# Optimization experiments

Measured on AMD Instinct MI355X. Metric: run time of the kernel, lower is better.

## Reference

```python
import jax, jax.numpy as jnp
import numpy as np


def setup_inputs() -> dict:
    key = jax.random.key(0)
    ks = jax.random.split(key, 9)
    B, C, H, W = 8, 512, 56, 56
    E = 256  # embed_dim = in_channels / r
    s = 0.02
    return {
        "x": jax.random.normal(ks[0], (B, C, H, W), dtype=jnp.float32),
        "wq": jax.random.normal(ks[1], (E, C), dtype=jnp.float32) * s,
        "bq": jax.random.normal(ks[2], (E,), dtype=jnp.float32) * s,
        "wk": jax.random.normal(ks[3], (E, C), dtype=jnp.float32) * s,
        "bk": jax.random.normal(ks[4], (E,), dtype=jnp.float32) * s,
        "wv": jax.random.normal(ks[5], (E, C), dtype=jnp.float32) * s,
        "bv": jax.random.normal(ks[6], (E,), dtype=jnp.float32) * s,
        "wo": jax.random.normal(ks[7], (C, E), dtype=jnp.float32) * s,
        "bo": jax.random.normal(ks[8], (C,), dtype=jnp.float32) * s,
    }


def reference(x, wq, bq, wk, bk, wv, bv, wo, bo):
    B, C, H, W = x.shape
    N = H * W
    # 1x1 convs == per-pixel linear projections; flatten spatial dims
    xf = x.reshape(B, C, N)                                   # b c n
    q = jnp.einsum("ec,bcn->bne", wq, xf) + bq                # b n e
    k = jnp.einsum("ec,bcn->ben", wk, xf) + bk[None, :, None] # b e n
    v = jnp.einsum("ec,bcn->bne", wv, xf) + bv                # b n e
    attn = jnp.einsum("bne,bem->bnm", q, k) / N               # b n n (unnormalized, /N scale)
    embed = jnp.einsum("bnm,bme->bne", attn, v)               # b n e
    out = jnp.einsum("ce,bne->bcn", wo, embed) + bo[None, :, None]
    return out.reshape(B, C, H, W) + x
```

## Files before the change

kernel.cpp:

```cpp
#include <hip/hip_runtime.h>
#include <hip/hip_bf16.h>


typedef __attribute__((ext_vector_type(8))) __bf16 bf16x8;
typedef __attribute__((ext_vector_type(4))) float floatx4;

struct __align__(8) bh4 { __hip_bfloat16 x, y, z, w; };
struct __align__(16) bh8 { __hip_bfloat16 h[8]; };

__device__ __forceinline__ void load_lds16(const void* g, void* l) {
    __builtin_amdgcn_global_load_lds((const __attribute__((address_space(1))) void*)g,
                                     (__attribute__((address_space(3))) void*)l, 16, 0, 0);
}

__global__ __launch_bounds__(256)
void prep_all(const float* __restrict__ wo, const float* __restrict__ wv,
              const float* __restrict__ wq, const float* __restrict__ wk,
              const float* __restrict__ bq, const float* __restrict__ bk,
              const float* __restrict__ bv,
              __hip_bfloat16* __restrict__ Pdb, __hip_bfloat16* __restrict__ Qtb,
              float* __restrict__ u, float* __restrict__ r, float* __restrict__ w,
              float* __restrict__ kap, float* __restrict__ sv)
{
    const int tid = threadIdx.x;
    if (blockIdx.z == 2) {
        int blk = blockIdx.y * 8 + blockIdx.x;
        if (blk < 2) {
            int c = blk * 256 + tid;
            float su = 0.f, sr = 0.f, sw = 0.f;
            for (int e = 0; e < 256; ++e) {
                su = fmaf(wo[(long long)c * 256 + e], bv[e], su);
                sr = fmaf(bk[e], wq[(long long)e * 512 + c], sr);
                sw = fmaf(wk[(long long)e * 512 + c], bq[e], sw);
            }
            u[c] = su; r[c] = sr; w[c] = sw;
            if (c == 0) {
                float k2 = 0.f;
                for (int e = 0; e < 256; ++e) k2 = fmaf(bk[e], bq[e], k2);
                *kap = k2;
            }
        } else if (blk == 2) {
            float4* p = (float4*)sv;
            for (int i = tid; i < 1024; i += 256) p[i] = make_float4(0.f, 0.f, 0.f, 0.f);
        }
        return;
    }
    __shared__ __align__(16) float As[16][68];
    __shared__ __align__(16) float Bs[16][68];
    const int tx = tid & 15, ty = tid >> 4;
    const int m0 = blockIdx.y * 64, n0 = blockIdx.x * 64;
    const bool doQ = (blockIdx.z == 1);
    const int lk = tid >> 4, lc = (tid & 15) * 4;
    const int lr = tid >> 2, lk4 = (tid & 3) * 4;
    float acc[4][4] = {};
    for (int k0 = 0; k0 < 256; k0 += 16) {
        float4 av, bv4;
        if (doQ) {
            av = *(const float4*)&wq[(long long)(k0 + lk) * 512 + m0 + lc];
            bv4 = *(const float4*)&wk[(long long)(k0 + lk) * 512 + n0 + lc];
        } else {
            av = *(const float4*)&wo[(long long)(m0 + lr) * 256 + k0 + lk4];
            bv4 = *(const float4*)&wv[(long long)(k0 + lk) * 512 + n0 + lc];
        }
        __syncthreads();
        if (doQ) {
            *(float4*)&As[lk][lc] = av;
        } else {
            As[lk4 + 0][lr] = av.x; As[lk4 + 1][lr] = av.y;
            As[lk4 + 2][lr] = av.z; As[lk4 + 3][lr] = av.w;
        }
        *(float4*)&Bs[lk][lc] = bv4;
        __syncthreads();
#pragma unroll
        for (int kk = 0; kk < 16; ++kk) {
            float a[4], b[4];
#pragma unroll
            for (int i = 0; i < 4; ++i) { a[i] = As[kk][ty * 4 + i]; b[i] = Bs[kk][tx * 4 + i]; }
#pragma unroll
            for (int i = 0; i < 4; ++i)
#pragma unroll
                for (int j = 0; j < 4; ++j) acc[i][j] = fmaf(a[i], b[j], acc[i][j]);
        }
    }
    const int mo = m0 + ty * 4, no = n0 + tx * 4;
    if (doQ) {
#pragma unroll
        for (int i = 0; i < 4; ++i)
#pragma unroll
            for (int j = 0; j < 4; ++j)
                Qtb[(long long)(mo + i) * 512 + no + j] = __float2bfloat16(acc[i][j]);
    } else {
#pragma unroll
        for (int i = 0; i < 4; ++i)
#pragma unroll
            for (int j = 0; j < 4; ++j) {
                __hip_bfloat16 v = __float2bfloat16(acc[i][j]);
                Pdb[(long long)(mo + i) * 1024 + no + j] = v;
                Pdb[(long long)(mo + i) * 1024 + no + j + 512] = v;
            }
    }
}

__global__ __launch_bounds__(256)
void transpose_conv(const float* __restrict__ x, __hip_bfloat16* __restrict__ xT,
                    __hip_bfloat16* __restrict__ xnp, float* __restrict__ s)
{
    __shared__ float t[64][65];
    const int b = blockIdx.z;
    const int n0 = blockIdx.x * 64, c0 = blockIdx.y * 64;
    const int tid = threadIdx.x;
    const int nch = tid & 7;
    const int cr  = tid >> 3;
    __hip_bfloat16* xTo = xT + (long long)b * 3200 * 512;
    __hip_bfloat16* xno = xnp + (long long)b * 512 * 3200;

    if (n0 >= 3136) {
        bh8 z8;
#pragma unroll
        for (int k = 0; k < 8; ++k) z8.h[k] = __float2bfloat16(0.f);
#pragma unroll
        for (int pass = 0; pass < 2; ++pass) {
            int rr = cr + 32 * pass;
            *(bh8*)&xno[(long long)(c0 + rr) * 3200 + n0 + nch * 8] = z8;
            *(bh8*)&xTo[(long long)(n0 + rr) * 512 + c0 + nch * 8] = z8;
        }
        return;
    }
    const float* xb = x + (long long)b * 512 * 3136;
#pragma unroll
    for (int pass = 0; pass < 2; ++pass) {
        const int cl = cr + 32 * pass;
        const int c = c0 + cl;
        const float* xr = xb + (long long)c * 3136 + n0 + nch * 8;
        float4 v0 = *(const float4*)xr;
        float4 v1 = *(const float4*)(xr + 4);
        bh8 o;
        o.h[0] = __float2bfloat16(v0.x); o.h[1] = __float2bfloat16(v0.y);
        o.h[2] = __float2bfloat16(v0.z); o.h[3] = __float2bfloat16(v0.w);
        o.h[4] = __float2bfloat16(v1.x); o.h[5] = __float2bfloat16(v1.y);
        o.h[6] = __float2bfloat16(v1.z); o.h[7] = __float2bfloat16(v1.w);
        *(bh8*)&xno[(long long)c * 3200 + n0 + nch * 8] = o;
        const int nl = nch * 8;
        t[nl + 0][cl] = v0.x; t[nl + 1][cl] = v0.y;
        t[nl + 2][cl] = v0.z; t[nl + 3][cl] = v0.w;
        t[nl + 4][cl] = v1.x; t[nl + 5][cl] = v1.y;
        t[nl + 6][cl] = v1.z; t[nl + 7][cl] = v1.w;
        float rs = v0.x + v0.y + v0.z + v0.w + v1.x + v1.y + v1.z + v1.w;
        rs += __shfl_xor(rs, 1, 8);
        rs += __shfl_xor(rs, 2, 8);
        rs += __shfl_xor(rs, 4, 8);
        if (nch == 0) atomicAdd(&s[b * 512 + c], rs);
    }
    __syncthreads();
#pragma unroll
    for (int pass = 0; pass < 2; ++pass) {
        const int nl = cr + 32 * pass;
        const int cc = nch * 8;
        bh8 o;
#pragma unroll
        for (int k = 0; k < 8; ++k) o.h[k] = __float2bfloat16(t[nl][cc + k]);
        *(bh8*)&xTo[(long long)(n0 + nl) * 512 + c0 + cc] = o;
    }
}

__global__ __launch_bounds__(256)
void vec2_kernel(const __hip_bfloat16* __restrict__ T, const __hip_bfloat16* __restrict__ Pdb,
                 const __hip_bfloat16* __restrict__ Qtb, const float* __restrict__ s,
                 const float* __restrict__ u, const float* __restrict__ w,
                 const float* __restrict__ kap, const float* __restrict__ bo,
                 float* __restrict__ ps, float* __restrict__ sq, float* __restrict__ a2)
{
    const int idx = blockIdx.x * 4 + (threadIdx.x >> 6);
    const int lane = threadIdx.x & 63;
    const int b = idx >> 9, c = idx & 511;
    const int j0 = lane * 8;
    const float* sb = s + b * 512;
    float4 s0 = *(const float4*)&sb[j0], s1 = *(const float4*)&sb[j0 + 4];
    float4 w0 = *(const float4*)&w[j0],  w1 = *(const float4*)&w[j0 + 4];
    bf16x8 pv = *(const bf16x8*)&Pdb[(long long)c * 1024 + j0];
    bf16x8 qv = *(const bf16x8*)&Qtb[(long long)c * 512 + j0];
    bf16x8 tv = *(const bf16x8*)&T[(long long)b * 262144 + (long long)c * 512 + j0];
    float sj[8] = {s0.x, s0.y, s0.z, s0.w, s1.x, s1.y, s1.z, s1.w};
    float wj[8] = {w0.x, w0.y, w0.z, w0.w, w1.x, w1.y, w1.z, w1.w};
    float aps = 0.f, asq = 0.f, atw = 0.f, asw = 0.f;
#pragma unroll
    for (int t = 0; t < 8; ++t) {
        aps = fmaf((float)pv[t], sj[t], aps);
        asq = fmaf((float)qv[t], sj[t], asq);
        atw = fmaf((float)tv[t], wj[t], atw);
        asw = fmaf(sj[t], wj[t], asw);
    }
#pragma unroll
    for (int m = 1; m < 64; m <<= 1) {
        aps += __shfl_xor(aps, m);
        asq += __shfl_xor(asq, m);
        atw += __shfl_xor(atw, m);
        asw += __shfl_xor(asw, m);
    }
    if (lane == 0) {
        ps[idx] = aps; sq[idx] = asq;
        float kp = *kap;
        a2[idx] = (atw + u[c] * asw + aps * kp) * (1.f / 3136.f) + u[c] * kp + bo[c];
    }
}

#define SWZ64(row) ((row) & 7)

__global__ __launch_bounds__(256)
void mfma_g(const __hip_bfloat16* __restrict__ A, long long sA, int lda,
            __hip_bfloat16* __restrict__ C, long long sC, int ldc,
            int kLen)
{
    constexpr int BKT = 64;
    constexpr int CPR = BKT / 8;
    constexpr int NC = 64 * CPR / 256;
    constexpr int LSZ = 64 * BKT;
    __shared__ __hip_bfloat16 As[2 * LSZ];
    __shared__ __hip_bfloat16 Bs[2 * LSZ];
    const int tid = threadIdx.x;
    const int lane = tid & 63;
    const int w = tid >> 6;
    const int wm = (w >> 1) << 5;
    const int wn = (w & 1) << 5;
    const int ln = lane & 15;
    const int hi = lane >> 4;
    const int bx = blockIdx.x;
    const int batch = bx & 7, ks = bx >> 3;
    int p = blockIdx.y, mt = 0;
    while (p >= 8 - mt) { p -= 8 - mt; ++mt; }
    const int nt = mt + p;
    const int m0 = mt << 6, n0 = nt << 6;
    const long long k0 = (long long)ks * kLen;

    const __hip_bfloat16* gA[NC];
    const __hip_bfloat16* gB[NC];
#pragma unroll
    for (int q0 = 0; q0 < NC; ++q0) {
        int q = tid + 256 * q0;
        int row = q / CPR;
        int c = (q % CPR) ^ SWZ64(row);
        gA[q0] = A + batch * sA + (long long)(m0 + row) * lda + k0 + c * 8;
        gB[q0] = A + batch * sA + (long long)(n0 + row) * lda + k0 + c * 8;
    }
    floatx4 acc[2][2] = {};
    const int nK = kLen / BKT;

#pragma unroll
    for (int q0 = 0; q0 < NC; ++q0) {
        load_lds16(gA[q0], As + (tid + 256 * q0) * 8);
        load_lds16(gB[q0], Bs + (tid + 256 * q0) * 8);
        gA[q0] += BKT; gB[q0] += BKT;
    }
    __syncthreads();

    int cur = 0;
    for (int kt = 0; kt < nK; ++kt) {
        if (kt + 1 < nK) {
            const int off = (cur ^ 1) * LSZ;
#pragma unroll
            for (int q0 = 0; q0 < NC; ++q0) {
                load_lds16(gA[q0], As + off + (tid + 256 * q0) * 8);
                load_lds16(gB[q0], Bs + off + (tid + 256 * q0) * 8);
                gA[q0] += BKT; gB[q0] += BKT;
            }
        }
        const __hip_bfloat16* Ac = As + cur * LSZ;
        const __hip_bfloat16* Bc = Bs + cur * LSZ;
#pragma unroll
        for (int kk = 0; kk < BKT / 32; ++kk) {
            const int cidx = kk * 4 + hi;
            bf16x8 af[2], bfr[2];
#pragma unroll
            for (int i = 0; i < 2; ++i) {
                int row = wm + i * 16 + ln;
                af[i] = *(const bf16x8*)(Ac + row * BKT + ((cidx ^ SWZ64(row)) << 3));
            }
#pragma unroll
            for (int j = 0; j < 2; ++j) {
                int row = wn + j * 16 + ln;
                bfr[j] = *(const bf16x8*)(Bc + row * BKT + ((cidx ^ SWZ64(row)) << 3));
            }
#pragma unroll
            for (int i = 0; i < 2; ++i)
#pragma unroll
                for (int j = 0; j < 2; ++j)
                    acc[i][j] = __builtin_amdgcn_mfma_f32_16x16x32_bf16(af[i], bfr[j], acc[i][j], 0, 0, 0);
        }
        if (kt + 1 < nK) {
            __syncthreads();
            cur ^= 1;
        }
    }

    __hip_bfloat16* Cb = C + batch * sC + ks * 512;
#pragma unroll
    for (int i = 0; i < 2; ++i) {
        int mb = m0 + wm + i * 16 + hi * 4;
#pragma unroll
        for (int j = 0; j < 2; ++j) {
            int nl = n0 + wn + j * 16 + ln;
            bh4 mv;
            mv.x = __float2bfloat16(acc[i][j][0]);
            mv.y = __float2bfloat16(acc[i][j][1]);
            mv.z = __float2bfloat16(acc[i][j][2]);
            mv.w = __float2bfloat16(acc[i][j][3]);
            Cb[(long long)(mb + 0) * ldc + nl] = mv.x;
            Cb[(long long)(mb + 1) * ldc + nl] = mv.y;
            Cb[(long long)(mb + 2) * ldc + nl] = mv.z;
            Cb[(long long)(mb + 3) * ldc + nl] = mv.w;
            if (mt != nt)
                *(bh4*)&Cb[(long long)nl * ldc + mb] = mv;
        }
    }
}

template<int MODE>
__global__ __launch_bounds__(256)
void mfma_sm(const __hip_bfloat16* __restrict__ A, long long sA, int lda,
             const __hip_bfloat16* __restrict__ B, long long sB, int ldb,
             __hip_bfloat16* __restrict__ C, long long sC, int ldc,
             const float* __restrict__ pu, const float* __restrict__ pr,
             const float* __restrict__ pps, const float* __restrict__ psq,
             int kLen)
{
    constexpr int BKT = 64;
    constexpr int CPR = BKT / 8;
    constexpr int NC = 64 * CPR / 256;
    constexpr int LSZ = 64 * BKT;
    __shared__ __hip_bfloat16 As[2 * LSZ];
    __shared__ __hip_bfloat16 Bs[2 * LSZ];
    const int tid = threadIdx.x;
    const int lane = tid & 63;
    const int w = tid >> 6;
    const int wm = (w >> 1) << 5;
    const int wn = (w & 1) << 5;
    const int ln = lane & 15;
    const int hi = lane >> 4;
    const int batch = blockIdx.x;
    const int m0 = blockIdx.z << 6;
    const int n0 = blockIdx.y << 6;

    const __hip_bfloat16* gA[NC];
    const __hip_bfloat16* gB[NC];
#pragma unroll
    for (int q0 = 0; q0 < NC; ++q0) {
        int q = tid + 256 * q0;
        int row = q / CPR;
        int c = (q % CPR) ^ SWZ64(row);
        gA[q0] = A + batch * sA + (long long)(m0 + row) * lda + c * 8;
        gB[q0] = B + batch * sB + (long long)(n0 + row) * ldb + c * 8;
    }
    floatx4 acc[2][2] = {};
    const int nK = kLen / BKT;

#pragma unroll
    for (int q0 = 0; q0 < NC; ++q0) {
        load_lds16(gA[q0], As + (tid + 256 * q0) * 8);
        load_lds16(gB[q0], Bs + (tid + 256 * q0) * 8);
        gA[q0] += BKT; gB[q0] += BKT;
    }
    __syncthreads();

    int cur = 0;
    for (int kt = 0; kt < nK; ++kt) {
        if (kt + 1 < nK) {
            const int off = (cur ^ 1) * LSZ;
#pragma unroll
            for (int q0 = 0; q0 < NC; ++q0) {
                load_lds16(gA[q0], As + off + (tid + 256 * q0) * 8);
                load_lds16(gB[q0], Bs + off + (tid + 256 * q0) * 8);
                gA[q0] += BKT; gB[q0] += BKT;
            }
        }
        const __hip_bfloat16* Ac = As + cur * LSZ;
        const __hip_bfloat16* Bc = Bs + cur * LSZ;
#pragma unroll
        for (int kk = 0; kk < BKT / 32; ++kk) {
            const int cidx = kk * 4 + hi;
            bf16x8 af[2], bfr[2];
#pragma unroll
            for (int i = 0; i < 2; ++i) {
                int row = wm + i * 16 + ln;
                af[i] = *(const bf16x8*)(Ac + row * BKT + ((cidx ^ SWZ64(row)) << 3));
            }
#pragma unroll
            for (int j = 0; j < 2; ++j) {
                int row = wn + j * 16 + ln;
                bfr[j] = *(const bf16x8*)(Bc + row * BKT + ((cidx ^ SWZ64(row)) << 3));
            }
#pragma unroll
            for (int i = 0; i < 2; ++i)
#pragma unroll
                for (int j = 0; j < 2; ++j)
                    acc[i][j] = __builtin_amdgcn_mfma_f32_16x16x32_bf16(af[i], bfr[j], acc[i][j], 0, 0, 0);
        }
        if (kt + 1 < nK) {
            __syncthreads();
            cur ^= 1;
        }
    }

    __hip_bfloat16* Cb = C + batch * sC;
#pragma unroll
    for (int i = 0; i < 2; ++i) {
        int mb = m0 + wm + i * 16 + hi * 4;
#pragma unroll
        for (int r = 0; r < 4; ++r) {
#pragma unroll
            for (int j = 0; j < 2; ++j) {
                int nl = n0 + wn + j * 16 + ln;
                float v = acc[i][j][r];
                if (MODE == 6) {
                    float uu = pu[mb + r], rr = pr[nl];
                    v = (v + uu * psq[batch * 512 + nl] + pps[batch * 512 + mb + r] * rr)
                        * (1.f / 3136.f) + uu * rr;
                }
                Cb[(long long)(mb + r) * ldc + nl] = __float2bfloat16(v);
            }
        }
    }
}

__global__ __launch_bounds__(256)
void mfma64(const __hip_bfloat16* __restrict__ A, long long sA, int lda,
            const __hip_bfloat16* __restrict__ B, long long sB, int ldb,
            float* __restrict__ C, long long sC, int ldc,
            const float* __restrict__ bias, int sBias,
            const float* __restrict__ xres, long long sX,
            int kLen, int Nreal)
{
    constexpr int BKT = 64;
    constexpr int CPR = BKT / 8;
    constexpr int NA = 64 * CPR / 256;
    constexpr int NB = 128 * CPR / 256;
    constexpr int LSA = 64 * BKT;
    constexpr int LSB = 128 * BKT;
    __shared__ __hip_bfloat16 As[2 * LSA];
    __shared__ __hip_bfloat16 Bs[2 * LSB];
    const int tid = threadIdx.x;
    const int lane = tid & 63;
    const int w = tid >> 6;
    const int ln = lane & 15;
    const int hi = lane >> 4;
    const int batch = blockIdx.x;
    const int m0 = blockIdx.z << 6;
    const int n0 = blockIdx.y << 7;

    const __hip_bfloat16* gA[NA];
    const __hip_bfloat16* gB[NB];
#pragma unroll
    for (int q0 = 0; q0 < NA; ++q0) {
        int q = tid + 256 * q0;
        int row = q / CPR;
        int c = (q % CPR) ^ SWZ64(row);
        gA[q0] = A + batch * sA + (long long)(m0 + row) * lda + c * 8;
    }
#pragma unroll
    for (int q0 = 0; q0 < NB; ++q0) {
        int q = tid + 256 * q0;
        int row = q / CPR;
        int c = (q % CPR) ^ SWZ64(row);
        gB[q0] = B + batch * sB + (long long)(n0 + row) * ldb + c * 8;
    }

    const float* xb = xres + batch * sX;
    float xr[4][4][2];

    floatx4 acc[4][2] = {};
    const int nK = kLen / BKT;

#pragma unroll
    for (int q0 = 0; q0 < NA; ++q0) {
        load_lds16(gA[q0], As + (tid + 256 * q0) * 8);
        gA[q0] += BKT;
    }
#pragma unroll
    for (int q0 = 0; q0 < NB; ++q0) {
        load_lds16(gB[q0], Bs + (tid + 256 * q0) * 8);
        gB[q0] += BKT;
    }
    __syncthreads();

    int cur = 0;
    for (int kt = 0; kt < nK; ++kt) {
        if (kt + 1 < nK) {
            const int offA = (cur ^ 1) * LSA;
            const int offB = (cur ^ 1) * LSB;
#pragma unroll
            for (int q0 = 0; q0 < NA; ++q0) {
                load_lds16(gA[q0], As + offA + (tid + 256 * q0) * 8);
                gA[q0] += BKT;
            }
#pragma unroll
            for (int q0 = 0; q0 < NB; ++q0) {
                load_lds16(gB[q0], Bs + offB + (tid + 256 * q0) * 8);
                gB[q0] += BKT;
            }
        } else {
#pragma unroll
            for (int i = 0; i < 4; ++i)
#pragma unroll
                for (int r = 0; r < 4; ++r)
#pragma unroll
                    for (int j = 0; j < 2; ++j) {
                        int mb = m0 + i * 16 + hi * 4 + r;
                        int nl = n0 + w * 32 + j * 16 + ln;
                        int nlc = nl < Nreal ? nl : Nreal - 1;
                        xr[i][r][j] = xb[(long long)mb * ldc + nlc];
                    }
        }
        const __hip_bfloat16* Ac = As + cur * LSA;
        const __hip_bfloat16* Bc = Bs + cur * LSB;
#pragma unroll
        for (int kk = 0; kk < BKT / 32; ++kk) {
            const int cidx = kk * 4 + hi;
            bf16x8 af[4], bfr[2];
#pragma unroll
            for (int i = 0; i < 4; ++i) {
                int row = i * 16 + ln;
                af[i] = *(const bf16x8*)(Ac + row * BKT + ((cidx ^ SWZ64(row)) << 3));
            }
#pragma unroll
            for (int j = 0; j < 2; ++j) {
                int row = w * 32 + j * 16 + ln;
                bfr[j] = *(const bf16x8*)(Bc + row * BKT + ((cidx ^ SWZ64(row)) << 3));
            }
#pragma unroll
            for (int i = 0; i < 4; ++i)
#pragma unroll
                for (int j = 0; j < 2; ++j)
                    acc[i][j] = __builtin_amdgcn_mfma_f32_16x16x32_bf16(af[i], bfr[j], acc[i][j], 0, 0, 0);
        }
        if (kt + 1 < nK) {
            __syncthreads();
            cur ^= 1;
        }
    }

    float* Cb = C + batch * sC;
#pragma unroll
    for (int i = 0; i < 4; ++i) {
        int mb = m0 + i * 16 + hi * 4;
#pragma unroll
        for (int r = 0; r < 4; ++r) {
            float bb = bias[batch * sBias + mb + r];
#pragma unroll
            for (int j = 0; j < 2; ++j) {
                int nl = n0 + w * 32 + j * 16 + ln;
                if (nl < Nreal) {
                    Cb[(long long)(mb + r) * ldc + nl] = acc[i][j][r] + bb + xr[i][r][j];
                }
            }
        }
    }
}

extern "C" void kernel_launch(void* const* d_in, const int* in_sizes, int n_in,
                              void* d_out, int out_size, void* d_ws, size_t ws_size,
                              hipStream_t stream)
{
    const float* x  = (const float*)d_in[0];
    const float* wq = (const float*)d_in[1];
    const float* bq = (const float*)d_in[2];
    const float* wk = (const float*)d_in[3];
    const float* bk = (const float*)d_in[4];
    const float* wv = (const float*)d_in[5];
    const float* bv = (const float*)d_in[6];
    const float* wo = (const float*)d_in[7];
    const float* bo = (const float*)d_in[8];
    float* out = (float*)d_out;

    const int N = 3136;
    const long long xs = 512LL * N;
    const long long xs2 = 512LL * 3200;

    char* ob = (char*)d_out;
    __hip_bfloat16* xnp = (__hip_bfloat16*)ob;
    __hip_bfloat16* Gp2 = (__hip_bfloat16*)(ob + 26214400);
    __hip_bfloat16* Tb  = (__hip_bfloat16*)(ob + 34603008);

    char* wsb = (char*)d_ws;
    __hip_bfloat16* xT  = (__hip_bfloat16*)wsb;
    __hip_bfloat16* A2b = (__hip_bfloat16*)(wsb + 26214400);
    __hip_bfloat16* Pdb = (__hip_bfloat16*)(wsb + 30408704);
    __hip_bfloat16* Qtb = (__hip_bfloat16*)(wsb + 31457280);
    float* sv  = (float*)(wsb + 31981568);
    float* u_  = (float*)(wsb + 31997952);
    float* r_  = (float*)(wsb + 32000000);
    float* w_  = (float*)(wsb + 32002048);
    float* kap = (float*)(wsb + 32004096);
    float* ps  = (float*)(wsb + 32004112);
    float* sq  = (float*)(wsb + 32020496);
    float* a2v = (float*)(wsb + 32036880);

    prep_all<<<dim3(8, 8, 3), 256, 0, stream>>>(wo, wv, wq, wk, bq, bk, bv,
                                                Pdb, Qtb, u_, r_, w_, kap, sv);

    transpose_conv<<<dim3(50, 8, 8), 256, 0, stream>>>(x, xT, xnp, sv);

    mfma_g<<<dim3(16, 36), 256, 0, stream>>>(
        xnp, xs2, 3200, Gp2, 524288, 1024, 1600);

    mfma_sm<5><<<dim3(8, 8, 8), 256, 0, stream>>>(
        Pdb, 0, 1024, Gp2, 524288, 1024, Tb, 262144, 512,
        nullptr, nullptr, nullptr, nullptr, 1024);

    vec2_kernel<<<1024, 256, 0, stream>>>(Tb, Pdb, Qtb, sv, u_, w_, kap, bo, ps, sq, a2v);

    mfma_sm<6><<<dim3(8, 8, 8), 256, 0, stream>>>(
        Tb, 262144, 512, Qtb, 0, 512, A2b, 262144, 512,
        u_, r_, ps, sq, 512);

    mfma64<<<dim3(8, 25, 8), 256, 0, stream>>>(
        A2b, 262144, 512, xT, 3200LL * 512, 512,
        out, xs, N, a2v, 512, x, xs, 512, N);
}
```

Before: 232.3 us.

## Drop LDS staging in mfma64 and load MFMA fragments directly from global

Removes the double-buffered shared-memory pipeline (global_load_lds plus barriers) from the output-projection GEMM. Each wave now reads its bf16x8 A and B fragments straight from global memory, unrolled by four, and the residual x values are loaded before the loop. This removes LDS traffic and synchronisation, but the A tile is re-read by all four waves through cache and the reads are less coalesced.

```diff
diff --git a/kernel.cpp b/kernel.cpp
--- a/kernel.cpp
+++ b/kernel.cpp
@@ -429,14 +429,6 @@
             const float* __restrict__ xres, long long sX,
             int kLen, int Nreal)
 {
-    constexpr int BKT = 64;
-    constexpr int CPR = BKT / 8;
-    constexpr int NA = 64 * CPR / 256;
-    constexpr int NB = 128 * CPR / 256;
-    constexpr int LSA = 64 * BKT;
-    constexpr int LSB = 128 * BKT;
-    __shared__ __hip_bfloat16 As[2 * LSA];
-    __shared__ __hip_bfloat16 Bs[2 * LSB];
     const int tid = threadIdx.x;
     const int lane = tid & 63;
     const int w = tid >> 6;
@@ -446,95 +438,45 @@
     const int m0 = blockIdx.z << 6;
     const int n0 = blockIdx.y << 7;
 
-    const __hip_bfloat16* gA[NA];
-    const __hip_bfloat16* gB[NB];
-#pragma unroll
-    for (int q0 = 0; q0 < NA; ++q0) {
-        int q = tid + 256 * q0;
-        int row = q / CPR;
-        int c = (q % CPR) ^ SWZ64(row);
-        gA[q0] = A + batch * sA + (long long)(m0 + row) * lda + c * 8;
-    }
-#pragma unroll
-    for (int q0 = 0; q0 < NB; ++q0) {
-        int q = tid + 256 * q0;
-        int row = q / CPR;
-        int c = (q % CPR) ^ SWZ64(row);
-        gB[q0] = B + batch * sB + (long long)(n0 + row) * ldb + c * 8;
-    }
+    const __hip_bfloat16* pa[4];
+#pragma unroll
+    for (int i = 0; i < 4; ++i)
+        pa[i] = A + batch * sA + (long long)(m0 + i * 16 + ln) * lda + hi * 8;
+    const __hip_bfloat16* pb[2];
+#pragma unroll
+    for (int j = 0; j < 2; ++j)
+        pb[j] = B + batch * sB + (long long)(n0 + w * 32 + j * 16 + ln) * ldb + hi * 8;
 
     const float* xb = xres + batch * sX;
     float xr[4][4][2];
+#pragma unroll
+    for (int i = 0; i < 4; ++i)
+#pragma unroll
+        for (int r = 0; r < 4; ++r)
+#pragma unroll
+            for (int j = 0; j < 2; ++j) {
+                int mb = m0 + i * 16 + hi * 4 + r;
+                int nl = n0 + w * 32 + j * 16 + ln;
+                int nlc = nl < Nreal ? nl : Nreal - 1;
+                xr[i][r][j] = xb[(long long)mb * ldc + nlc];
+            }
 
     floatx4 acc[4][2] = {};
-    const int nK = kLen / BKT;
-
-#pragma unroll
-    for (int q0 = 0; q0 < NA; ++q0) {
-        load_lds16(gA[q0], As + (tid + 256 * q0) * 8);
-        gA[q0] += BKT;
-    }
-#pragma unroll
-    for (int q0 = 0; q0 < NB; ++q0) {
-        load_lds16(gB[q0], Bs + (tid + 256 * q0) * 8);
-        gB[q0] += BKT;
-    }
-    __syncthreads();
-
-    int cur = 0;
-    for (int kt = 0; kt < nK; ++kt) {
-        if (kt + 1 < nK) {
-            const int offA = (cur ^ 1) * LSA;
-            const int offB = (cur ^ 1) * LSB;
-#pragma unroll
-            for (int q0 = 0; q0 < NA; ++q0) {
-                load_lds16(gA[q0], As + offA + (tid + 256 * q0) * 8);
-                gA[q0] += BKT;
-            }
-#pragma unroll
-            for (int q0 = 0; q0 < NB; ++q0) {
-                load_lds16(gB[q0], Bs + offB + (tid + 256 * q0) * 8);
-                gB[q0] += BKT;
-            }
-        } else {
-#pragma unroll
-            for (int i = 0; i < 4; ++i)
-#pragma unroll
-                for (int r = 0; r < 4; ++r)
-#pragma unroll
-                    for (int j = 0; j < 2; ++j) {
-                        int mb = m0 + i * 16 + hi * 4 + r;
-                        int nl = n0 + w * 32 + j * 16 + ln;
-                        int nlc = nl < Nreal ? nl : Nreal - 1;
-                        xr[i][r][j] = xb[(long long)mb * ldc + nlc];
-                    }
-        }
-        const __hip_bfloat16* Ac = As + cur * LSA;
-        const __hip_bfloat16* Bc = Bs + cur * LSB;
-#pragma unroll
-        for (int kk = 0; kk < BKT / 32; ++kk) {
-            const int cidx = kk * 4 + hi;
-            bf16x8 af[4], bfr[2];
-#pragma unroll
-            for (int i = 0; i < 4; ++i) {
-                int row = i * 16 + ln;
-                af[i] = *(const bf16x8*)(Ac + row * BKT + ((cidx ^ SWZ64(row)) << 3));
-            }
-#pragma unroll
-            for (int j = 0; j < 2; ++j) {
-                int row = w * 32 + j * 16 + ln;
-                bfr[j] = *(const bf16x8*)(Bc + row * BKT + ((cidx ^ SWZ64(row)) << 3));
-            }
-#pragma unroll
-            for (int i = 0; i < 4; ++i)
-#pragma unroll
-                for (int j = 0; j < 2; ++j)
-                    acc[i][j] = __builtin_amdgcn_mfma_f32_16x16x32_bf16(af[i], bfr[j], acc[i][j], 0, 0, 0);
-        }
-        if (kt + 1 < nK) {
-            __syncthreads();
-            cur ^= 1;
-        }
+    const int nK = kLen / 32;
+#pragma unroll 4
+    for (int kc = 0; kc < nK; ++kc) {
+        bf16x8 af[4], bfr[2];
+#pragma unroll
+        for (int i = 0; i < 4; ++i)
+            af[i] = *(const bf16x8*)(pa[i] + kc * 32);
+#pragma unroll
+        for (int j = 0; j < 2; ++j)
+            bfr[j] = *(const bf16x8*)(pb[j] + kc * 32);
+#pragma unroll
+        for (int i = 0; i < 4; ++i)
+#pragma unroll
+            for (int j = 0; j < 2; ++j)
+                acc[i][j] = __builtin_amdgcn_mfma_f32_16x16x32_bf16(af[i], bfr[j], acc[i][j], 0, 0, 0);
     }
 
     float* Cb = C + batch * sC;
```

Measured after the change: 284.6 us. +22.5%, slower.

## Use partial vmcnt waits with raw barriers in GEMMs; single-buffer mfma64 LDS

Applied to the files above, without the earlier changes.

In the two 64x64 GEMM kernels, the full __syncthreads after each prefetch is replaced by an s_waitcnt vmcnt(4) plus a raw s_barrier, so the current tile's async LDS loads are awaited while the next tile's loads stay in flight. In mfma64 the double-buffered LDS is removed in favour of a single buffer with load, sync, compute, sync, and the residual x loads are hoisted to kernel start. This halves LDS use in mfma64, which may raise occupancy, but that kernel loses load/compute overlap within a block. The hard-coded vmcnt count must match the number of outstanding loads per thread.

```diff
diff --git a/kernel.cpp b/kernel.cpp
--- a/kernel.cpp
+++ b/kernel.cpp
@@ -251,7 +251,6 @@
         load_lds16(gB[q0], Bs + (tid + 256 * q0) * 8);
         gA[q0] += BKT; gB[q0] += BKT;
     }
-    __syncthreads();
 
     int cur = 0;
     for (int kt = 0; kt < nK; ++kt) {
@@ -263,7 +262,11 @@
                 load_lds16(gB[q0], Bs + off + (tid + 256 * q0) * 8);
                 gA[q0] += BKT; gB[q0] += BKT;
             }
-        }
+            asm volatile("s_waitcnt vmcnt(4)" ::: "memory");
+        } else {
+            asm volatile("s_waitcnt vmcnt(0)" ::: "memory");
+        }
+        __builtin_amdgcn_s_barrier();
         const __hip_bfloat16* Ac = As + cur * LSZ;
         const __hip_bfloat16* Bc = Bs + cur * LSZ;
 #pragma unroll
@@ -287,7 +290,7 @@
                     acc[i][j] = __builtin_amdgcn_mfma_f32_16x16x32_bf16(af[i], bfr[j], acc[i][j], 0, 0, 0);
         }
         if (kt + 1 < nK) {
-            __syncthreads();
+            __builtin_amdgcn_s_barrier();
             cur ^= 1;
         }
     }
@@ -359,7 +362,6 @@
         load_lds16(gB[q0], Bs + (tid + 256 * q0) * 8);
         gA[q0] += BKT; gB[q0] += BKT;
     }
-    __syncthreads();
 
     int cur = 0;
     for (int kt = 0; kt < nK; ++kt) {
@@ -371,7 +373,11 @@
                 load_lds16(gB[q0], Bs + off + (tid + 256 * q0) * 8);
                 gA[q0] += BKT; gB[q0] += BKT;
             }
-        }
+            asm volatile("s_waitcnt vmcnt(4)" ::: "memory");
+        } else {
+            asm volatile("s_waitcnt vmcnt(0)" ::: "memory");
+        }
+        __builtin_amdgcn_s_barrier();
         const __hip_bfloat16* Ac = As + cur * LSZ;
         const __hip_bfloat16* Bc = Bs + cur * LSZ;
 #pragma unroll
@@ -395,7 +401,7 @@
                     acc[i][j] = __builtin_amdgcn_mfma_f32_16x16x32_bf16(af[i], bfr[j], acc[i][j], 0, 0, 0);
         }
         if (kt + 1 < nK) {
-            __syncthreads();
+            __builtin_amdgcn_s_barrier();
             cur ^= 1;
         }
     }
@@ -433,10 +439,8 @@
     constexpr int CPR = BKT / 8;
     constexpr int NA = 64 * CPR / 256;
     constexpr int NB = 128 * CPR / 256;
-    constexpr int LSA = 64 * BKT;
-    constexpr int LSB = 128 * BKT;
-    __shared__ __hip_bfloat16 As[2 * LSA];
-    __shared__ __hip_bfloat16 Bs[2 * LSB];
+    __shared__ __hip_bfloat16 As[64 * BKT];
+    __shared__ __hip_bfloat16 Bs[128 * BKT];
     const int tid = threadIdx.x;
     const int lane = tid & 63;
     const int w = tid >> 6;
@@ -465,52 +469,32 @@
 
     const float* xb = xres + batch * sX;
     float xr[4][4][2];
+#pragma unroll
+    for (int i = 0; i < 4; ++i)
+#pragma unroll
+        for (int r = 0; r < 4; ++r)
+#pragma unroll
+            for (int j = 0; j < 2; ++j) {
+                int mb = m0 + i * 16 + hi * 4 + r;
+                int nl = n0 + w * 32 + j * 16 + ln;
+                int nlc = nl < Nreal ? nl : Nreal - 1;
+                xr[i][r][j] = xb[(long long)mb * ldc + nlc];
+            }
 
     floatx4 acc[4][2] = {};
     const int nK = kLen / BKT;
-
-#pragma unroll
-    for (int q0 = 0; q0 < NA; ++q0) {
-        load_lds16(gA[q0], As + (tid + 256 * q0) * 8);
-        gA[q0] += BKT;
-    }
-#pragma unroll
-    for (int q0 = 0; q0 < NB; ++q0) {
-        load_lds16(gB[q0], Bs + (tid + 256 * q0) * 8);
-        gB[q0] += BKT;
-    }
-    __syncthreads();
-
-    int cur = 0;
     for (int kt = 0; kt < nK; ++kt) {
-        if (kt + 1 < nK) {
-            const int offA = (cur ^ 1) * LSA;
-            const int offB = (cur ^ 1) * LSB;
-#pragma unroll
-            for (int q0 = 0; q0 < NA; ++q0) {
-                load_lds16(gA[q0], As + offA + (tid + 256 * q0) * 8);
-                gA[q0] += BKT;
-            }
-#pragma unroll
-            for (int q0 = 0; q0 < NB; ++q0) {
-                load_lds16(gB[q0], Bs + offB + (tid + 256 * q0) * 8);
-                gB[q0] += BKT;
-            }
-        } else {
-#pragma unroll
-            for (int i = 0; i < 4; ++i)
-#pragma unroll
-                for (int r = 0; r < 4; ++r)
-#pragma unroll
-                    for (int j = 0; j < 2; ++j) {
-                        int mb = m0 + i * 16 + hi * 4 + r;
-                        int nl = n0 + w * 32 + j * 16 + ln;
-                        int nlc = nl < Nreal ? nl : Nreal - 1;
-                        xr[i][r][j] = xb[(long long)mb * ldc + nlc];
-                    }
-        }
-        const __hip_bfloat16* Ac = As + cur * LSA;
-        const __hip_bfloat16* Bc = Bs + cur * LSB;
+#pragma unroll
+        for (int q0 = 0; q0 < NA; ++q0) {
+            load_lds16(gA[q0], As + (tid + 256 * q0) * 8);
+            gA[q0] += BKT;
+        }
+#pragma unroll
+        for (int q0 = 0; q0 < NB; ++q0) {
+            load_lds16(gB[q0], Bs + (tid + 256 * q0) * 8);
+            gB[q0] += BKT;
+        }
+        __syncthreads();
 #pragma unroll
         for (int kk = 0; kk < BKT / 32; ++kk) {
             const int cidx = kk * 4 + hi;
@@ -518,12 +502,12 @@
 #pragma unroll
             for (int i = 0; i < 4; ++i) {
                 int row = i * 16 + ln;
-                af[i] = *(const bf16x8*)(Ac + row * BKT + ((cidx ^ SWZ64(row)) << 3));
+                af[i] = *(const bf16x8*)(As + row * BKT + ((cidx ^ SWZ64(row)) << 3));
             }
 #pragma unroll
             for (int j = 0; j < 2; ++j) {
                 int row = w * 32 + j * 16 + ln;
-                bfr[j] = *(const bf16x8*)(Bc + row * BKT + ((cidx ^ SWZ64(row)) << 3));
+                bfr[j] = *(const bf16x8*)(Bs + row * BKT + ((cidx ^ SWZ64(row)) << 3));
             }
 #pragma unroll
             for (int i = 0; i < 4; ++i)
@@ -531,10 +515,7 @@
                 for (int j = 0; j < 2; ++j)
                     acc[i][j] = __builtin_amdgcn_mfma_f32_16x16x32_bf16(af[i], bfr[j], acc[i][j], 0, 0, 0);
         }
-        if (kt + 1 < nK) {
-            __syncthreads();
-            cur ^= 1;
-        }
+        __syncthreads();
     }
 
     float* Cb = C + batch * sC;
```

Result: no change. 228.6 us (-1.6%).
